# Kernel optimization log

Measured on AMD Instinct MI355X. Metric: run time of the kernel, lower is better.

Reference implementation:

```python
import jax, jax.numpy as jnp
import numpy as np
import math

N_LEVELS = 16
F_PER_LEVEL = 2
LOG2_T = 19
T = 1 << LOG2_T
BASE_RES = 16
MAX_RES = 2048
PER_LEVEL_SCALE = (MAX_RES / BASE_RES) ** (1.0 / (N_LEVELS - 1))
BOUND = 0.5
PRIMES = (np.uint32(1), np.uint32(2654435761), np.uint32(805459861))


def _weight_norm(v, g):
    # w = g * v / ||v||_row (torch weight_norm over dim=1)
    return v * (g / jnp.linalg.norm(v, axis=1))[:, None]


def _softplus100(x):
    # torch Softplus(beta=100)
    return jax.nn.softplus(100.0 * x) * 0.01


def hashgrid_encode(x01, table):
    # x01: [N,3] in [0,1]; table: [L, T, F]
    feats = []
    for l in range(N_LEVELS):
        scale = BASE_RES * (PER_LEVEL_SCALE ** l) - 1.0  # tcnn grid scale
        res = int(math.ceil(scale)) + 1
        pos = x01 * scale + 0.5
        pos_floor = jnp.floor(pos)
        w = pos - pos_floor                      # [N,3] trilinear fracs
        c0 = pos_floor.astype(jnp.uint32)        # [N,3] base corner
        dense = (res ** 3) <= T                  # static per level
        acc = jnp.zeros((x01.shape[0], F_PER_LEVEL), dtype=table.dtype)
        for corner in range(8):
            off = [(corner >> d) & 1 for d in range(3)]
            cx = c0[:, 0] + np.uint32(off[0])
            cy = c0[:, 1] + np.uint32(off[1])
            cz = c0[:, 2] + np.uint32(off[2])
            if dense:
                idx = cx + cy * np.uint32(res) + cz * np.uint32(res * res)
            else:
                idx = (cx * PRIMES[0]) ^ (cy * PRIMES[1]) ^ (cz * PRIMES[2])
                idx = idx & np.uint32(T - 1)
            wc = ((w[:, 0] if off[0] else 1.0 - w[:, 0])
                  * (w[:, 1] if off[1] else 1.0 - w[:, 1])
                  * (w[:, 2] if off[2] else 1.0 - w[:, 2]))
            acc = acc + wc[:, None] * table[l, idx.astype(jnp.int32)]
        feats.append(acc)
    return jnp.concatenate(feats, axis=-1)  # [N, 32]


def setup_inputs() -> dict:
    key = jax.random.key(0)
    ks = jax.random.split(key, 4)
    N = 2 ** 21
    x = jax.random.uniform(ks[0], (N, 3), jnp.float32, -BOUND, BOUND)
    table = jax.random.uniform(ks[1], (N_LEVELS, T, F_PER_LEVEL), jnp.float32, -1e-4, 1e-4)
    d_in, d_hid, d_out = 35, 64, 13
    v1 = jax.random.normal(ks[2], (d_hid, d_in), jnp.float32) * (math.sqrt(2) / math.sqrt(d_hid))
    v2 = jax.random.normal(ks[3], (d_out, d_hid), jnp.float32) * 1e-4 + math.sqrt(math.pi) / math.sqrt(d_hid)
    g1 = jnp.linalg.norm(v1, axis=1)
    g2 = jnp.linalg.norm(v2, axis=1)
    b1 = jnp.zeros((d_hid,), jnp.float32)
    b2 = jnp.full((d_out,), -0.5, jnp.float32)  # -sphere_init_radius
    return {"x": x, "table": table, "v1": v1, "g1": g1, "b1": b1,
            "v2": v2, "g2": g2, "b2": b2}


def reference(x, table, v1, g1, b1, v2, g2, b2):
    x01 = jnp.clip((x + BOUND) / (2.0 * BOUND), 0.0, 1.0)
    enc = hashgrid_encode(x01, table)            # [N, 32]
    h = jnp.concatenate([x, enc], axis=1)        # [N, 35]
    w1 = _weight_norm(v1, g1)
    w2 = _weight_norm(v2, g2)
    h = _softplus100(h @ w1.T + b1)
    out = h @ w2.T + b2                          # [N, 13]
    return out
```

## Files before the change

kernel.cpp:

```cpp
#include <hip/hip_runtime.h>
#include <hip/hip_fp16.h>
#include <cstdint>
#include <cmath>

#define NLEV 16
#define NHASH 11
#define NDENSE 5
#define TBL (1u << 19)
#define NBKT 32768

typedef _Float16 half8 __attribute__((ext_vector_type(8)));
typedef float f32x4 __attribute__((ext_vector_type(4)));

struct LevelParams {
    float scale[NLEV];
    uint32_t res[NLEV];
    uint32_t hashed_mask;
};

__device__ __forceinline__ int krow_map(int kr) {
    if (kr <= 2) return kr;
    if (kr >= 4 && kr <= 13) return kr - 1;
    if (kr >= 16 && kr <= 37) return kr - 3;
    return -1;
}

__global__ __launch_bounds__(256) void prep_weights(
    const float* __restrict__ v1, const float* __restrict__ g1,
    const float* __restrict__ v2, const float* __restrict__ g2,
    float* __restrict__ w1t, float* __restrict__ w2n,
    __half* __restrict__ w1f, __half* __restrict__ w2f)
{
    int t = threadIdx.x;
    if (t < 64) {
        float s = 0.f;
        #pragma unroll
        for (int k = 0; k < 35; ++k) { float v = v1[t*35 + k]; s += v*v; }
        float f = g1[t] / sqrtf(s);
        #pragma unroll
        for (int k = 0; k < 35; ++k) w1t[k*64 + t] = v1[t*35 + k] * f;
    } else if (t < 77) {
        int r = t - 64;
        float s = 0.f;
        #pragma unroll
        for (int k = 0; k < 64; ++k) { float v = v2[r*64 + k]; s += v*v; }
        float f = g2[r] / sqrtf(s);
        #pragma unroll
        for (int k = 0; k < 64; ++k) w2n[r*64 + k] = v2[r*64 + k] * f;
    }
    __syncthreads();
    for (int i = t; i < 4096; i += 256) {
        int j = i & 7, lane = (i >> 3) & 63, nt = (i >> 9) & 3, kc = i >> 11;
        int kr = kc*32 + ((lane >> 4) << 3) + j;
        int ncol = nt*16 + (lane & 15);
        int m = krow_map(kr);
        float val = (m >= 0) ? w1t[m*64 + ncol] : 0.f;
        w1f[i] = __float2half(val);
    }
    for (int i = t; i < 1024; i += 256) {
        int j = i & 7, lane = (i >> 3) & 63, kc = i >> 9;
        int kr = kc*32 + ((lane >> 4) << 3) + j;
        int col = lane & 15;
        float val = (col < 13) ? w2n[col*64 + kr] : 0.f;
        w2f[i] = __float2half(val);
    }
}

__device__ __forceinline__ uint32_t bucket_key(float u0, float u1, float u2)
{
    uint32_t a = min(31u, (uint32_t)(u0 * 32.f));
    uint32_t b = min(31u, (uint32_t)(u1 * 32.f));
    uint32_t c = min(31u, (uint32_t)(u2 * 32.f));
    return (a << 10) | (b << 5) | c;
}

__device__ __forceinline__ void load_u(const float* __restrict__ x, int pp,
                                       float& u0, float& u1, float& u2)
{
    float x0 = x[3*(size_t)pp + 0];
    float x1 = x[3*(size_t)pp + 1];
    float x2 = x[3*(size_t)pp + 2];
    u0 = fminf(fmaxf(x0 + 0.5f, 0.f), 1.f);
    u1 = fminf(fmaxf(x1 + 0.5f, 0.f), 1.f);
    u2 = fminf(fmaxf(x2 + 0.5f, 0.f), 1.f);
}

__global__ __launch_bounds__(256) void pack_and_hist(
    const float2* __restrict__ tin, uint32_t* __restrict__ tout, int n_entries,
    const float* __restrict__ x, uint32_t* __restrict__ hist, int N,
    int packBlocks)
{
    int b = blockIdx.x;
    if (b < packBlocks) {
        int i = b * 256 + threadIdx.x;
        if (i < n_entries) {
            float2 v = tin[i];
            __half2 h = __floats2half2_rn(v.x, v.y);
            tout[i] = *reinterpret_cast<uint32_t*>(&h);
        }
    } else {
        int i = (b - packBlocks) * 256 + threadIdx.x;
        if (i < N) {
            float u0, u1, u2;
            load_u(x, i, u0, u1, u2);
            atomicAdd(&hist[bucket_key(u0, u1, u2)], 1u);
        }
    }
}

__global__ __launch_bounds__(1024) void scan_hist(
    const uint32_t* __restrict__ hist, uint32_t* __restrict__ offs)
{
    __shared__ uint32_t part[1024];
    int t = threadIdx.x;
    uint32_t loc[32];
    uint32_t s = 0;
    #pragma unroll
    for (int k = 0; k < 32; ++k) { loc[k] = s; s += hist[t*32 + k]; }
    part[t] = s;
    __syncthreads();
    for (int d = 1; d < 1024; d <<= 1) {
        uint32_t v = (t >= d) ? part[t - d] : 0u;
        __syncthreads();
        part[t] += v;
        __syncthreads();
    }
    uint32_t base = (t > 0) ? part[t - 1] : 0u;
    #pragma unroll
    for (int k = 0; k < 32; ++k) offs[t*32 + k] = base + loc[k];
}

__global__ __launch_bounds__(256) void scatter_kernel(
    const float* __restrict__ x, uint32_t* __restrict__ offs,
    float4* __restrict__ xs4, int N)
{
    int i = blockIdx.x * 256 + threadIdx.x;
    if (i < N) {
        float x0 = x[3*(size_t)i + 0];
        float x1 = x[3*(size_t)i + 1];
        float x2 = x[3*(size_t)i + 2];
        float u0 = fminf(fmaxf(x0 + 0.5f, 0.f), 1.f);
        float u1 = fminf(fmaxf(x1 + 0.5f, 0.f), 1.f);
        float u2 = fminf(fmaxf(x2 + 0.5f, 0.f), 1.f);
        uint32_t pos = atomicAdd(&offs[bucket_key(u0, u1, u2)], 1u);
        xs4[pos] = make_float4(x0, x1, x2, __int_as_float(i));
    }
}

__device__ __forceinline__ void encode_one(
    float u0, float u1, float u2, float s, uint32_t res, bool hashed,
    const uint32_t* __restrict__ tl, float& a0, float& a1)
{
    float px = u0 * s + 0.5f;
    float py = u1 * s + 0.5f;
    float pz = u2 * s + 0.5f;
    float fx = floorf(px), fy = floorf(py), fz = floorf(pz);
    float wx1 = px - fx, wy1 = py - fy, wz1 = pz - fz;
    float wx0 = 1.f - wx1, wy0 = 1.f - wy1, wz0 = 1.f - wz1;
    uint32_t cx = (uint32_t)fx, cy = (uint32_t)fy, cz = (uint32_t)fz;

    uint32_t ix0, ix1, iy0, iy1, iz0, iz1;
    if (hashed) {
        ix0 = cx;                 ix1 = cx + 1u;
        iy0 = cy * 2654435761u;   iy1 = (cy + 1u) * 2654435761u;
        iz0 = cz * 805459861u;    iz1 = (cz + 1u) * 805459861u;
    } else {
        ix0 = cx;                 ix1 = cx + 1u;
        iy0 = cy * res;           iy1 = iy0 + res;
        uint32_t rr = res * res;
        iz0 = cz * rr;            iz1 = iz0 + rr;
    }

    uint32_t idxs[8];
    #pragma unroll
    for (int c = 0; c < 8; ++c) {
        uint32_t jx = (c & 1) ? ix1 : ix0;
        uint32_t jy = (c & 2) ? iy1 : iy0;
        uint32_t jz = (c & 4) ? iz1 : iz0;
        idxs[c] = hashed ? ((jx ^ jy ^ jz) & (TBL - 1u)) : (jx + jy + jz);
    }
    uint32_t raw[8];
    #pragma unroll
    for (int c = 0; c < 8; ++c) raw[c] = tl[idxs[c]];

    float wxy00 = wx0*wy0, wxy10 = wx1*wy0, wxy01 = wx0*wy1, wxy11 = wx1*wy1;
    a0 = 0.f; a1 = 0.f;
    #pragma unroll
    for (int c = 0; c < 8; ++c) {
        float wxy = (c & 2) ? ((c & 1) ? wxy11 : wxy01)
                            : ((c & 1) ? wxy10 : wxy00);
        float w = wxy * ((c & 4) ? wz1 : wz0);
        __half2 hv = *reinterpret_cast<__half2*>(&raw[c]);
        float2 v = __half22float2(hv);
        a0 += w * v.x;
        a1 += w * v.y;
    }
}

template <int SORTED>
__global__ __launch_bounds__(256) void encode_hashed(
    const float* __restrict__ x, const float4* __restrict__ xs4,
    const uint32_t* __restrict__ tpk,
    uint32_t* __restrict__ feats, int N, int chunks_per_level, int lbase,
    LevelParams P)
{
    int bid = blockIdx.x;
    int ll = bid / chunks_per_level;
    int l = lbase + ll;
    int li = l - NDENSE;
    int base = (bid - ll * chunks_per_level) * 512 + threadIdx.x;
    const uint32_t* tl = tpk + (size_t)l * TBL;
    float s = P.scale[l];

    int p[2] = { base, base + 256 };
    uint2 Q[2][4];
    uint32_t par[2];
    float wx0[2], wx1[2], wyz[2][4];

    #pragma unroll
    for (int t = 0; t < 2; ++t) {
        int pp = (p[t] < N) ? p[t] : (N - 1);
        float u0, u1, u2;
        if (SORTED) {
            float4 v4 = xs4[pp];
            u0 = fminf(fmaxf(v4.x + 0.5f, 0.f), 1.f);
            u1 = fminf(fmaxf(v4.y + 0.5f, 0.f), 1.f);
            u2 = fminf(fmaxf(v4.z + 0.5f, 0.f), 1.f);
        } else {
            load_u(x, pp, u0, u1, u2);
        }

        float px = u0 * s + 0.5f;
        float py = u1 * s + 0.5f;
        float pz = u2 * s + 0.5f;
        float fx = floorf(px), fy = floorf(py), fz = floorf(pz);
        float a1f = px - fx, b1f = py - fy, c1f = pz - fz;
        wx1[t] = a1f; wx0[t] = 1.f - a1f;
        float wy0 = 1.f - b1f, wz0 = 1.f - c1f;
        uint32_t cx = (uint32_t)fx, cy = (uint32_t)fy, cz = (uint32_t)fz;

        wyz[t][0] = wy0 * wz0;
        wyz[t][1] = b1f * wz0;
        wyz[t][2] = wy0 * c1f;
        wyz[t][3] = b1f * c1f;

        uint32_t hy0 = cy * 2654435761u, hy1 = (cy + 1u) * 2654435761u;
        uint32_t hz0 = cz * 805459861u,  hz1 = (cz + 1u) * 805459861u;
        uint32_t r[4] = { hy0 ^ hz0, hy1 ^ hz0, hy0 ^ hz1, hy1 ^ hz1 };

        par[t] = 0u;
        if (!(cx & 1u)) {
            #pragma unroll
            for (int k = 0; k < 4; ++k) {
                uint32_t v0 = (cx ^ r[k]) & (TBL - 1u);
                Q[t][k] = *reinterpret_cast<const uint2*>(tl + (v0 & ~1u));
                par[t] |= (v0 & 1u) << k;
            }
        } else {
            #pragma unroll
            for (int k = 0; k < 4; ++k) {
                uint32_t v0 = (cx ^ r[k]) & (TBL - 1u);
                uint32_t v1 = ((cx + 1u) ^ r[k]) & (TBL - 1u);
                Q[t][k].x = tl[v0];
                Q[t][k].y = tl[v1];
            }
        }
    }

    #pragma unroll
    for (int t = 0; t < 2; ++t) {
        float a0 = 0.f, a1 = 0.f;
        #pragma unroll
        for (int k = 0; k < 4; ++k) {
            uint32_t swap = (par[t] >> k) & 1u;
            uint32_t b0 = swap ? Q[t][k].y : Q[t][k].x;
            uint32_t b1 = swap ? Q[t][k].x : Q[t][k].y;
            __half2 h0 = *reinterpret_cast<__half2*>(&b0);
            __half2 h1 = *reinterpret_cast<__half2*>(&b1);
            float2 c0 = __half22float2(h0);
            float2 c1 = __half22float2(h1);
            a0 += wyz[t][k] * (wx0[t] * c0.x + wx1[t] * c1.x);
            a1 += wyz[t][k] * (wx0[t] * c0.y + wx1[t] * c1.y);
        }
        __half2 hv = __floats2half2_rn(a0, a1);
        if (p[t] < N) {
            __builtin_nontemporal_store(*reinterpret_cast<uint32_t*>(&hv),
                                        &feats[(size_t)li * N + p[t]]);
        }
    }
}

__global__ __launch_bounds__(256) void mlp_mfma(
    const float4* __restrict__ xs4,
    const uint32_t* __restrict__ tpk,
    const uint32_t* __restrict__ feats,
    const __half* __restrict__ w1f,
    const __half* __restrict__ w2f,
    const float* __restrict__ b1,
    const float* __restrict__ b2,
    float* __restrict__ out, int N, LevelParams P)
{
    __shared__ uint4 ldsA[4][576];
    __shared__ int   ldsI[4][64];
    int wid = threadIdx.x >> 6, lane = threadIdx.x & 63;
    int wpt = blockIdx.x * 256 + wid * 64;
    int pt = wpt + lane;
    int pp = (pt < N) ? pt : (N - 1);

    float4 v4 = xs4[pp];
    float x0 = v4.x, x1 = v4.y, x2 = v4.z;
    ldsI[wid][lane] = __float_as_int(v4.w);
    float u0 = fminf(fmaxf(x0 + 0.5f, 0.f), 1.f);
    float u1 = fminf(fmaxf(x1 + 0.5f, 0.f), 1.f);
    float u2 = fminf(fmaxf(x2 + 0.5f, 0.f), 1.f);

    uint32_t dw[32];
    #pragma unroll
    for (int i = 0; i < 32; ++i) dw[i] = 0u;
    __half2 h01 = __floats2half2_rn(x0, x1);
    __half2 h2_ = __floats2half2_rn(x2, 0.f);
    dw[0] = *reinterpret_cast<uint32_t*>(&h01);
    dw[1] = *reinterpret_cast<uint32_t*>(&h2_);
    #pragma unroll
    for (int l = 0; l < NDENSE; ++l) {
        const uint32_t* tl = tpk + (size_t)l * TBL;
        float a0, a1;
        encode_one(u0, u1, u2, P.scale[l], P.res[l], false, tl, a0, a1);
        __half2 hv = __floats2half2_rn(a0, a1);
        dw[2 + l] = *reinterpret_cast<uint32_t*>(&hv);
    }
    #pragma unroll
    for (int li = 0; li < NHASH; ++li)
        dw[8 + li] = feats[(size_t)li * N + pp];

    #pragma unroll
    for (int c = 0; c < 8; ++c) {
        uint4 ch = make_uint4(dw[4*c], dw[4*c+1], dw[4*c+2], dw[4*c+3]);
        ldsA[wid][c*64 + lane] = ch;
    }

    const uint4* w1f4 = (const uint4*)w1f;
    half8 bf[4][2];
    #pragma unroll
    for (int nt = 0; nt < 4; ++nt)
        #pragma unroll
        for (int kc = 0; kc < 2; ++kc) {
            uint4 u = w1f4[(kc*4 + nt)*64 + lane];
            bf[nt][kc] = __builtin_bit_cast(half8, u);
        }

    f32x4 C[4][4];
    #pragma unroll
    for (int nt = 0; nt < 4; ++nt) {
        float bv = b1[nt*16 + (lane & 15)];
        #pragma unroll
        for (int m = 0; m < 4; ++m) C[m][nt] = f32x4{bv, bv, bv, bv};
    }

    #pragma unroll
    for (int m = 0; m < 4; ++m) {
        uint4 ua0 = ldsA[wid][((lane >> 4)      )*64 + m*16 + (lane & 15)];
        uint4 ua1 = ldsA[wid][((lane >> 4) + 4  )*64 + m*16 + (lane & 15)];
        half8 a0 = __builtin_bit_cast(half8, ua0);
        half8 a1 = __builtin_bit_cast(half8, ua1);
        #pragma unroll
        for (int nt = 0; nt < 4; ++nt) {
            C[m][nt] = __builtin_amdgcn_mfma_f32_16x16x32_f16(a0, bf[nt][0], C[m][nt], 0, 0, 0);
            C[m][nt] = __builtin_amdgcn_mfma_f32_16x16x32_f16(a1, bf[nt][1], C[m][nt], 0, 0, 0);
        }
    }

    #pragma unroll
    for (int m = 0; m < 4; ++m)
        #pragma unroll
        for (int nt = 0; nt < 4; ++nt)
            #pragma unroll
            for (int r = 0; r < 4; ++r) {
                float z = 100.f * C[m][nt][r];
                float t = __expf(-fabsf(z));
                C[m][nt][r] = (fmaxf(z, 0.f) + __logf(1.f + t)) * 0.01f;
            }

    uint32_t* hl = (uint32_t*)&ldsA[wid][0];
    bool evenl = (lane & 1) == 0;
    #pragma unroll
    for (int m = 0; m < 4; ++m)
        #pragma unroll
        for (int nt = 0; nt < 4; ++nt)
            #pragma unroll
            for (int r = 0; r < 4; ++r) {
                float self = C[m][nt][r];
                float other = __shfl_xor(self, 1);
                if (evenl) {
                    __half2 hp = __floats2half2_rn(self, other);
                    int prow = m*16 + ((lane >> 4) << 2) + r;
                    int colp = (nt*16 + (lane & 15)) >> 1;
                    hl[prow*36 + colp] = *reinterpret_cast<uint32_t*>(&hp);
                }
            }

    const uint4* w2f4 = (const uint4*)w2f;
    half8 b2f[2];
    #pragma unroll
    for (int kc = 0; kc < 2; ++kc) {
        uint4 u = w2f4[kc*64 + lane];
        b2f[kc] = __builtin_bit_cast(half8, u);
    }
    int col = lane & 15;
    float b2v = (col < 13) ? b2[col] : 0.f;

    #pragma unroll
    for (int m = 0; m < 4; ++m) {
        uint4 ua0 = ldsA[wid][(m*16 + col)*9 + 0 + (lane >> 4)];
        uint4 ua1 = ldsA[wid][(m*16 + col)*9 + 4 + (lane >> 4)];
        f32x4 c2 = f32x4{b2v, b2v, b2v, b2v};
        c2 = __builtin_amdgcn_mfma_f32_16x16x32_f16(
                 __builtin_bit_cast(half8, ua0), b2f[0], c2, 0, 0, 0);
        c2 = __builtin_amdgcn_mfma_f32_16x16x32_f16(
                 __builtin_bit_cast(half8, ua1), b2f[1], c2, 0, 0, 0);
        #pragma unroll
        for (int r = 0; r < 4; ++r) {
            int prow = m*16 + ((lane >> 4) << 2) + r;
            if (col < 13 && wpt + prow < N) {
                int og = ldsI[wid][prow];
                out[(size_t)og * 13 + col] = c2[r];
            }
        }
    }
}

__global__ __launch_bounds__(256) void mlp_dense_scalar(
    const float* __restrict__ x, const uint32_t* __restrict__ tpk,
    const uint32_t* __restrict__ feats,
    const float* __restrict__ w1t, const float* __restrict__ b1,
    const float* __restrict__ w2, const float* __restrict__ b2,
    float* __restrict__ out, int N, LevelParams P)
{
    int p = blockIdx.x * 256 + threadIdx.x;
    bool valid = (p < N);
    int pp = valid ? p : (N - 1);

    float x0 = x[3*(size_t)pp + 0];
    float x1 = x[3*(size_t)pp + 1];
    float x2 = x[3*(size_t)pp + 2];
    float u0 = fminf(fmaxf(x0 + 0.5f, 0.f), 1.f);
    float u1 = fminf(fmaxf(x1 + 0.5f, 0.f), 1.f);
    float u2 = fminf(fmaxf(x2 + 0.5f, 0.f), 1.f);

    uint32_t rf[NHASH];
    #pragma unroll
    for (int li = 0; li < NHASH; ++li) rf[li] = feats[(size_t)li * N + pp];

    float h[64];
    #pragma unroll
    for (int j = 0; j < 64; ++j)
        h[j] = b1[j] + x0 * w1t[0*64 + j] + x1 * w1t[1*64 + j] + x2 * w1t[2*64 + j];

    #pragma unroll
    for (int l = 0; l < NDENSE; ++l) {
        const uint32_t* tl = tpk + (size_t)l * TBL;
        float a0, a1;
        encode_one(u0, u1, u2, P.scale[l], P.res[l], false, tl, a0, a1);
        const float* c0p = w1t + (3 + 2*l) * 64;
        const float* c1p = c0p + 64;
        #pragma unroll
        for (int j = 0; j < 64; ++j) h[j] += a0 * c0p[j] + a1 * c1p[j];
    }
    #pragma unroll
    for (int li = 0; li < NHASH; ++li) {
        __half2 hv = *reinterpret_cast<__half2*>(&rf[li]);
        float2 f = __half22float2(hv);
        int l = li + NDENSE;
        const float* c0p = w1t + (3 + 2*l) * 64;
        const float* c1p = c0p + 64;
        #pragma unroll
        for (int j = 0; j < 64; ++j) h[j] += f.x * c0p[j] + f.y * c1p[j];
    }
    #pragma unroll
    for (int j = 0; j < 64; ++j) {
        float z = 100.f * h[j];
        float t = __expf(-fabsf(z));
        h[j] = (fmaxf(z, 0.f) + __logf(1.f + t)) * 0.01f;
    }
    float* op = out + (size_t)pp * 13;
    for (int o = 0; o < 13; ++o) {
        float a = b2[o];
        const float* wr = w2 + o * 64;
        #pragma unroll
        for (int k = 0; k < 64; ++k) a = fmaf(h[k], wr[k], a);
        if (valid) op[o] = a;
    }
}

template <int PACKED>
__global__ __launch_bounds__(256) void sdf_fused(
    const float* __restrict__ x, const void* __restrict__ table,
    const float* __restrict__ w1t, const float* __restrict__ b1,
    const float* __restrict__ w2, const float* __restrict__ b2,
    float* __restrict__ out, int N, LevelParams P)
{
    int i = blockIdx.x * 256 + threadIdx.x;
    bool valid = (i < N);
    int ii = valid ? i : (N - 1);

    float x0 = x[3*(size_t)ii + 0];
    float x1 = x[3*(size_t)ii + 1];
    float x2 = x[3*(size_t)ii + 2];
    float u0 = fminf(fmaxf(x0 + 0.5f, 0.f), 1.f);
    float u1 = fminf(fmaxf(x1 + 0.5f, 0.f), 1.f);
    float u2 = fminf(fmaxf(x2 + 0.5f, 0.f), 1.f);

    float h[64];
    #pragma unroll
    for (int j = 0; j < 64; ++j)
        h[j] = b1[j] + x0 * w1t[0*64 + j] + x1 * w1t[1*64 + j] + x2 * w1t[2*64 + j];

    for (int l = 0; l < NLEV; ++l) {
        bool hashed = (P.hashed_mask >> l) & 1u;
        float a0, a1;
        if (PACKED) {
            const uint32_t* tl = (const uint32_t*)table + (size_t)l * TBL;
            encode_one(u0, u1, u2, P.scale[l], P.res[l], hashed, tl, a0, a1);
        } else {
            const float* tl = (const float*)table + (size_t)l * (size_t)(TBL * 2u);
            float s = P.scale[l]; uint32_t res = P.res[l];
            float px = u0*s + 0.5f, py = u1*s + 0.5f, pz = u2*s + 0.5f;
            float fx = floorf(px), fy = floorf(py), fz = floorf(pz);
            float wx1 = px-fx, wy1 = py-fy, wz1 = pz-fz;
            float wx0 = 1.f-wx1, wy0 = 1.f-wy1, wz0 = 1.f-wz1;
            uint32_t cx = (uint32_t)fx, cy = (uint32_t)fy, cz = (uint32_t)fz;
            a0 = 0.f; a1 = 0.f;
            #pragma unroll
            for (int c = 0; c < 8; ++c) {
                uint32_t jx = cx + (c & 1);
                uint32_t jy = cy + ((c >> 1) & 1);
                uint32_t jz = cz + ((c >> 2) & 1);
                uint32_t idx = hashed
                    ? ((jx ^ (jy * 2654435761u) ^ (jz * 805459861u)) & (TBL - 1u))
                    : (jx + jy * res + jz * res * res);
                float w = ((c & 1) ? wx1 : wx0) * ((c & 2) ? wy1 : wy0)
                        * ((c & 4) ? wz1 : wz0);
                float2 v = *reinterpret_cast<const float2*>(tl + (size_t)idx * 2u);
                a0 += w * v.x; a1 += w * v.y;
            }
        }
        const float* c0p = w1t + (3 + 2*l) * 64;
        const float* c1p = c0p + 64;
        #pragma unroll
        for (int j = 0; j < 64; ++j) h[j] += a0 * c0p[j] + a1 * c1p[j];
    }

    #pragma unroll
    for (int j = 0; j < 64; ++j) {
        float z = 100.f * h[j];
        float t = __expf(-fabsf(z));
        h[j] = (fmaxf(z, 0.f) + __logf(1.f + t)) * 0.01f;
    }

    float* op = out + (size_t)ii * 13;
    for (int o = 0; o < 13; ++o) {
        float a = b2[o];
        const float* wr = w2 + o * 64;
        #pragma unroll
        for (int k = 0; k < 64; ++k) a += h[k] * wr[k];
        if (valid) op[o] = a;
    }
}

extern "C" void kernel_launch(void* const* d_in, const int* in_sizes, int n_in,
                              void* d_out, int out_size, void* d_ws, size_t ws_size,
                              hipStream_t stream)
{
    const float* x     = (const float*)d_in[0];
    const float* table = (const float*)d_in[1];
    const float* v1    = (const float*)d_in[2];
    const float* g1    = (const float*)d_in[3];
    const float* b1    = (const float*)d_in[4];
    const float* v2    = (const float*)d_in[5];
    const float* g2    = (const float*)d_in[6];
    const float* b2    = (const float*)d_in[7];
    float* out = (float*)d_out;
    int N = in_sizes[0] / 3;

    const int n_entries = NLEV * (int)TBL;
    const size_t packed_bytes = (size_t)n_entries * 4u;
    const size_t xs4_bytes    = (size_t)N * 16u;
    const size_t feats_bytes  = (size_t)NHASH * (size_t)N * 4u;
    const size_t hist_bytes   = (size_t)NBKT * 4u;
    const size_t w_bytes      = (35*64 + 13*64) * sizeof(float);
    const size_t wf_bytes     = (4096 + 1024) * sizeof(__half);

    size_t off_packed = 0;
    size_t off_xs4    = off_packed + packed_bytes;
    size_t off_feats  = off_xs4 + xs4_bytes;
    size_t off_hist   = off_feats + feats_bytes;
    size_t off_offs   = off_hist + hist_bytes;
    size_t off_w      = off_offs + hist_bytes;
    size_t off_wf     = off_w + w_bytes;
    size_t sorted_need = off_wf + wf_bytes;

    bool sorted_ok = (ws_size >= sorted_need);
    bool two_pass  = (ws_size >= packed_bytes + feats_bytes + w_bytes + wf_bytes);
    bool packed_ok = (ws_size >= packed_bytes + w_bytes + wf_bytes);

    uint32_t* tpk   = (uint32_t*)((char*)d_ws + off_packed);
    float4*   xs4   = (float4*)((char*)d_ws + off_xs4);
    uint32_t* hist  = (uint32_t*)((char*)d_ws + off_hist);
    uint32_t* offs  = (uint32_t*)((char*)d_ws + off_offs);
    uint32_t* feats;
    float* w1t;
    if (sorted_ok) {
        feats = (uint32_t*)((char*)d_ws + off_feats);
        w1t = (float*)((char*)d_ws + off_w);
    } else if (two_pass) {
        feats = (uint32_t*)((char*)d_ws + packed_bytes);
        w1t = (float*)((char*)d_ws + packed_bytes + feats_bytes);
    } else {
        feats = nullptr;
        w1t = (float*)((char*)d_ws + (packed_ok ? packed_bytes : 0));
    }
    float* w2n = w1t + 35 * 64;
    __half* w1f = (__half*)(w2n + 13 * 64);
    __half* w2f = w1f + 4096;

    LevelParams P;
    P.hashed_mask = 0u;
    double pls = pow(128.0, 1.0 / 15.0);
    for (int l = 0; l < NLEV; ++l) {
        double sc = 16.0 * pow(pls, (double)l) - 1.0;
        P.scale[l] = (float)sc;
        uint32_t res = (uint32_t)(ceil(sc)) + 1u;
        P.res[l] = res;
        uint64_t r3 = (uint64_t)res * res * res;
        if (r3 > (uint64_t)TBL) P.hashed_mask |= (1u << l);
    }

    prep_weights<<<1, 256, 0, stream>>>(v1, g1, v2, g2, w1t, w2n, w1f, w2f);

    int chunks = (N + 255) / 256;
    int packBlocks = (n_entries + 255) / 256;
    if (sorted_ok) {
        hipMemsetAsync(hist, 0, hist_bytes, stream);
        pack_and_hist<<<packBlocks + chunks, 256, 0, stream>>>(
            (const float2*)table, tpk, n_entries, x, hist, N, packBlocks);
        scan_hist<<<1, 1024, 0, stream>>>(hist, offs);
        scatter_kernel<<<chunks, 256, 0, stream>>>(x, offs, xs4, N);
        int chunks2 = (N + 511) / 512;
        encode_hashed<1><<<chunks2 * 6, 256, 0, stream>>>(
            x, xs4, tpk, feats, N, chunks2, 5, P);
        encode_hashed<1><<<chunks2 * 5, 256, 0, stream>>>(
            x, xs4, tpk, feats, N, chunks2, 11, P);
        mlp_mfma<<<chunks, 256, 0, stream>>>(
            xs4, tpk, feats, w1f, w2f, b1, b2, out, N, P);
    } else if (two_pass) {
        pack_and_hist<<<packBlocks, 256, 0, stream>>>(
            (const float2*)table, tpk, n_entries, x, nullptr, 0, packBlocks);
        int chunks2 = (N + 511) / 512;
        encode_hashed<0><<<chunks2 * NHASH, 256, 0, stream>>>(
            x, nullptr, tpk, feats, N, chunks2, 5, P);
        mlp_dense_scalar<<<chunks, 256, 0, stream>>>(
            x, tpk, feats, w1t, b1, w2n, b2, out, N, P);
    } else if (packed_ok) {
        pack_and_hist<<<packBlocks, 256, 0, stream>>>(
            (const float2*)table, tpk, n_entries, x, nullptr, 0, packBlocks);
        sdf_fused<1><<<chunks, 256, 0, stream>>>(
            x, (const void*)tpk, w1t, b1, w2n, b2, out, N, P);
    } else {
        sdf_fused<0><<<chunks, 256, 0, stream>>>(
            x, (const void*)table, w1t, b1, w2n, b2, out, N, P);
    }
}
```

Before: 746.2 us.

## Refine spatial sort to 64^3 buckets and overlay histogram on feats buffer

```diff
diff --git a/kernel.cpp b/kernel.cpp
--- a/kernel.cpp
+++ b/kernel.cpp
@@ -7,7 +7,7 @@
 #define NHASH 11
 #define NDENSE 5
 #define TBL (1u << 19)
-#define NBKT 32768
+#define NBKT 262144
 
 typedef _Float16 half8 __attribute__((ext_vector_type(8)));
 typedef float f32x4 __attribute__((ext_vector_type(4)));
@@ -68,10 +68,10 @@
 
 __device__ __forceinline__ uint32_t bucket_key(float u0, float u1, float u2)
 {
-    uint32_t a = min(31u, (uint32_t)(u0 * 32.f));
-    uint32_t b = min(31u, (uint32_t)(u1 * 32.f));
-    uint32_t c = min(31u, (uint32_t)(u2 * 32.f));
-    return (a << 10) | (b << 5) | c;
+    uint32_t a = min(63u, (uint32_t)(u0 * 64.f));
+    uint32_t b = min(63u, (uint32_t)(u1 * 64.f));
+    uint32_t c = min(63u, (uint32_t)(u2 * 64.f));
+    return (a << 12) | (b << 6) | c;
 }
 
 __device__ __forceinline__ void load_u(const float* __restrict__ x, int pp,
@@ -113,10 +113,8 @@
 {
     __shared__ uint32_t part[1024];
     int t = threadIdx.x;
-    uint32_t loc[32];
     uint32_t s = 0;
-    #pragma unroll
-    for (int k = 0; k < 32; ++k) { loc[k] = s; s += hist[t*32 + k]; }
+    for (int k = 0; k < 256; ++k) s += hist[t*256 + k];
     part[t] = s;
     __syncthreads();
     for (int d = 1; d < 1024; d <<= 1) {
@@ -126,8 +124,11 @@
         __syncthreads();
     }
     uint32_t base = (t > 0) ? part[t - 1] : 0u;
-    #pragma unroll
-    for (int k = 0; k < 32; ++k) offs[t*32 + k] = base + loc[k];
+    for (int k = 0; k < 256; ++k) {
+        uint32_t h = hist[t*256 + k];
+        offs[t*256 + k] = base;
+        base += h;
+    }
 }
 
 __global__ __launch_bounds__(256) void scatter_kernel(
@@ -201,14 +202,12 @@
 __global__ __launch_bounds__(256) void encode_hashed(
     const float* __restrict__ x, const float4* __restrict__ xs4,
     const uint32_t* __restrict__ tpk,
-    uint32_t* __restrict__ feats, int N, int chunks_per_level, int lbase,
-    LevelParams P)
+    uint32_t* __restrict__ feats, int N, int chunks_per_level, LevelParams P)
 {
     int bid = blockIdx.x;
-    int ll = bid / chunks_per_level;
-    int l = lbase + ll;
-    int li = l - NDENSE;
-    int base = (bid - ll * chunks_per_level) * 512 + threadIdx.x;
+    int li = bid / chunks_per_level;
+    int l = li + NDENSE;
+    int base = (bid - li * chunks_per_level) * 512 + threadIdx.x;
     const uint32_t* tl = tpk + (size_t)l * TBL;
     float s = P.scale[l];
 
@@ -593,20 +592,17 @@
     size_t off_packed = 0;
     size_t off_xs4    = off_packed + packed_bytes;
     size_t off_feats  = off_xs4 + xs4_bytes;
-    size_t off_hist   = off_feats + feats_bytes;
-    size_t off_offs   = off_hist + hist_bytes;
-    size_t off_w      = off_offs + hist_bytes;
+    size_t off_w      = off_feats + feats_bytes;
     size_t off_wf     = off_w + w_bytes;
     size_t sorted_need = off_wf + wf_bytes;
-
-    bool sorted_ok = (ws_size >= sorted_need);
+    bool overlay_ok = feats_bytes >= 2 * hist_bytes;
+
+    bool sorted_ok = (ws_size >= sorted_need) && overlay_ok;
     bool two_pass  = (ws_size >= packed_bytes + feats_bytes + w_bytes + wf_bytes);
     bool packed_ok = (ws_size >= packed_bytes + w_bytes + wf_bytes);
 
     uint32_t* tpk   = (uint32_t*)((char*)d_ws + off_packed);
     float4*   xs4   = (float4*)((char*)d_ws + off_xs4);
-    uint32_t* hist  = (uint32_t*)((char*)d_ws + off_hist);
-    uint32_t* offs  = (uint32_t*)((char*)d_ws + off_offs);
     uint32_t* feats;
     float* w1t;
     if (sorted_ok) {
@@ -619,6 +615,8 @@
         feats = nullptr;
         w1t = (float*)((char*)d_ws + (packed_ok ? packed_bytes : 0));
     }
+    uint32_t* hist = feats;
+    uint32_t* offs = feats + NBKT;
     float* w2n = w1t + 35 * 64;
     __half* w1f = (__half*)(w2n + 13 * 64);
     __half* w2f = w1f + 4096;
@@ -646,10 +644,8 @@
         scan_hist<<<1, 1024, 0, stream>>>(hist, offs);
         scatter_kernel<<<chunks, 256, 0, stream>>>(x, offs, xs4, N);
         int chunks2 = (N + 511) / 512;
-        encode_hashed<1><<<chunks2 * 6, 256, 0, stream>>>(
-            x, xs4, tpk, feats, N, chunks2, 5, P);
-        encode_hashed<1><<<chunks2 * 5, 256, 0, stream>>>(
-            x, xs4, tpk, feats, N, chunks2, 11, P);
+        encode_hashed<1><<<chunks2 * NHASH, 256, 0, stream>>>(
+            x, xs4, tpk, feats, N, chunks2, P);
         mlp_mfma<<<chunks, 256, 0, stream>>>(
             xs4, tpk, feats, w1f, w2f, b1, b2, out, N, P);
     } else if (two_pass) {
@@ -657,7 +653,7 @@
             (const float2*)table, tpk, n_entries, x, nullptr, 0, packBlocks);
         int chunks2 = (N + 511) / 512;
         encode_hashed<0><<<chunks2 * NHASH, 256, 0, stream>>>(
-            x, nullptr, tpk, feats, N, chunks2, 5, P);
+            x, nullptr, tpk, feats, N, chunks2, P);
         mlp_dense_scalar<<<chunks, 256, 0, stream>>>(
             x, tpk, feats, w1t, b1, w2n, b2, out, N, P);
     } else if (packed_ok) {
```

Measured after the change: 841.9 us. 12.8% more time.
